# Kernel tuning notes

Hardware: AMD Instinct MI355X
Metric: run time of the kernel (lower is better)

## Reference

```python
import jax, jax.numpy as jnp
import numpy as np

N = 1024          # number of junctions
H = 1024          # heatmap height
W = 1024          # heatmap width
NUM_SAMPLES = 64  # samples along each candidate segment (torch_sampler)
DETECT_THRESH = 0.5
INLIER_THRESH = 0.99


def setup_inputs() -> dict:
    key = jax.random.key(0)
    k1, k2 = jax.random.split(key)
    # junctions are (h, w) float coordinates inside the image
    junctions = jax.random.uniform(k1, (N, 2), dtype=jnp.float32) * (H - 1)
    heatmap = jax.random.uniform(k2, (H, W), dtype=jnp.float32)
    return {"junctions": junctions, "heatmap": heatmap}


def _bilinear_sample(heatmap, ch, cw):
    """SOLD2 detect_bilinear: gather 4 corners, bilinear weights. ch/cw: [N,N,S]."""
    hf = jnp.floor(ch); hc = jnp.ceil(ch)
    wf = jnp.floor(cw); wc = jnp.ceil(cw)
    hfi = hf.astype(jnp.int32); hci = hc.astype(jnp.int32)
    wfi = wf.astype(jnp.int32); wci = wc.astype(jnp.int32)
    return (heatmap[hfi, wfi] * (hc - ch) * (wc - cw)
          + heatmap[hfi, wci] * (hc - ch) * (cw - wf)
          + heatmap[hci, wfi] * (ch - hf) * (wc - cw)
          + heatmap[hci, wci] * (ch - hf) * (cw - wf))


def reference(junctions, heatmap):
    n = junctions.shape[0]
    Hh, Ww = heatmap.shape
    t = jnp.linspace(0.0, 1.0, NUM_SAMPLES, dtype=jnp.float32)  # [S]
    # cand_samples[i, j, s] = junc[i] * t[s] + junc[j] * (1 - t[s])  (start=i, end=j)
    ch = junctions[:, None, 0:1] * t + junctions[None, :, 0:1] * (1.0 - t)  # [N,N,S]
    cw = junctions[:, None, 1:2] * t + junctions[None, :, 1:2] * (1.0 - t)  # [N,N,S]
    ch = jnp.clip(ch, 0.0, Hh - 1)
    cw = jnp.clip(cw, 0.0, Ww - 1)
    feat = _bilinear_sample(heatmap, ch, cw)                    # [N,N,S]
    mean_feat = feat.mean(axis=-1)                              # [N,N]
    inlier_ratio = (feat > DETECT_THRESH).astype(jnp.float32).mean(axis=-1)
    # candidate map: strict upper triangle (torch.triu(ones, diagonal=1))
    cand_mask = jnp.triu(jnp.ones((n, n), dtype=bool), k=1)
    detected = (mean_feat > DETECT_THRESH) & (inlier_ratio >= INLIER_THRESH) & cand_mask
    line_map = (detected | detected.T).astype(jnp.int32)        # symmetric line map
    return line_map, mean_feat
```

## Files before the change

### kernel.cpp

```cpp
#include <hip/hip_runtime.h>

#define NJ 1024
#define DETECT 0.5f
#define RESCUE 0.4975f

__device__ __forceinline__ float sample_t(int s) {
    return (s == 63) ? 1.0f : (float)s * (1.0f / 63.0f);
}

__device__ __forceinline__ void exact_pair(const float2 ja, const float2 jb,
                                           const float* __restrict__ heat,
                                           float& mean_o, float& min_o)
{
    float acc = 0.0f;
    float mn  = __builtin_inff();
    for (int s = 0; s < 64; ++s) {
        const float t  = sample_t(s);
        const float om = 1.0f - t;
        float ch = __fadd_rn(__fmul_rn(ja.x, t), __fmul_rn(jb.x, om));
        float cw = __fadd_rn(__fmul_rn(ja.y, t), __fmul_rn(jb.y, om));
        ch = fminf(fmaxf(ch, 0.0f), 1023.0f);
        cw = fminf(fmaxf(cw, 0.0f), 1023.0f);
        const float hf = floorf(ch), hc = ceilf(ch);
        const float wf = floorf(cw), wc = ceilf(cw);
        const int hfi = (int)hf, hci = (int)hc;
        const int wfi = (int)wf, wci = (int)wc;
        const float a00 = heat[(hfi << 10) + wfi];
        const float a01 = heat[(hfi << 10) + wci];
        const float a10 = heat[(hci << 10) + wfi];
        const float a11 = heat[(hci << 10) + wci];
        const float t1 = __fmul_rn(__fmul_rn(a00, __fsub_rn(hc, ch)), __fsub_rn(wc, cw));
        const float t2 = __fmul_rn(__fmul_rn(a01, __fsub_rn(hc, ch)), __fsub_rn(cw, wf));
        const float t3 = __fmul_rn(__fmul_rn(a10, __fsub_rn(ch, hf)), __fsub_rn(wc, cw));
        const float t4 = __fmul_rn(__fmul_rn(a11, __fsub_rn(ch, hf)), __fsub_rn(cw, wf));
        const float feat = __fadd_rn(__fadd_rn(__fadd_rn(t1, t2), t3), t4);
        acc += feat;
        mn = fminf(mn, feat);
    }
    mean_o = acc * (1.0f / 64.0f);
    min_o  = mn;
}

__global__ __launch_bounds__(256) void pack_kernel(
    const float* __restrict__ heat, uint4* __restrict__ packed4,
    const float* __restrict__ junc,
    float* __restrict__ line_out, float* __restrict__ mean_out)
{
    const int idx = blockIdx.x * 256 + threadIdx.x;
    const int h = idx >> 8;
    const int w4 = (idx & 255) << 2;
    const int hn = (h < 1023) ? h + 1 : 1023;
    const float* r0 = heat + (h  << 10);
    const float* r1 = heat + (hn << 10);
    const float4 a = *(const float4*)(r0 + w4);
    const float4 b = *(const float4*)(r1 + w4);
    const int wnext = (w4 + 4 <= 1023) ? w4 + 4 : 1023;
    const float a4 = r0[wnext];
    const float b4 = r1[wnext];

    const float av[5] = {a.x, a.y, a.z, a.w, a4};
    const float bv[5] = {b.x, b.y, b.z, b.w, b4};
    unsigned int out[4];
    #pragma unroll
    for (int u = 0; u < 4; ++u) {
        const unsigned int c0 = (unsigned int)__float2int_rn(av[u]     * 255.0f);
        const unsigned int c1 = (unsigned int)__float2int_rn(av[u + 1] * 255.0f);
        const unsigned int c2 = (unsigned int)__float2int_rn(bv[u]     * 255.0f);
        const unsigned int c3 = (unsigned int)__float2int_rn(bv[u + 1] * 255.0f);
        out[u] = c0 | (c1 << 8) | (c2 << 16) | (c3 << 24);
    }
    packed4[idx] = make_uint4(out[0], out[1], out[2], out[3]);

    if (threadIdx.x == 0) {
        const int r = blockIdx.x;
        const float2 jr = ((const float2*)junc)[r];
        float mean, mnv;
        exact_pair(jr, jr, heat, mean, mnv);
        const int p = (r << 10) + r;
        mean_out[p] = mean;
        line_out[p] = 0.0f;
    }
}

__global__ __launch_bounds__(256) void sold2_thread_kernel(
    const float* __restrict__ junc,
    const float* __restrict__ heat,
    const unsigned int* __restrict__ packed,
    float* __restrict__ line_out,
    float* __restrict__ mean_out)
{
    const int q = blockIdx.x * 256 + threadIdx.x;
    const int r = q >> 9;
    const int c = (q & 511) + 1;
    const int j = (r + c) & 1023;

    const float2 jr  = ((const float2*)junc)[r];
    const float2 jjc = ((const float2*)junc)[j];

    float acc = 0.0f;
    float mn  = __builtin_inff();

    #pragma unroll
    for (int s0 = 0; s0 < 64; s0 += 16) {
        float chv[16], cwv[16];
        unsigned int cv[16];
        #pragma unroll
        for (int u = 0; u < 16; ++u) {
            const int s = s0 + u;
            const float t  = sample_t(s);
            const float om = 1.0f - t;
            float ch = __fadd_rn(__fmul_rn(jr.x, t), __fmul_rn(jjc.x, om));
            float cw = __fadd_rn(__fmul_rn(jr.y, t), __fmul_rn(jjc.y, om));
            ch = fminf(fmaxf(ch, 0.0f), 1023.0f);
            cw = fminf(fmaxf(cw, 0.0f), 1023.0f);
            chv[u] = ch;
            cwv[u] = cw;
            const int hfi = (int)ch;
            const int wfi = (int)cw;
            cv[u] = packed[(hfi << 10) + wfi];
        }
        #pragma unroll
        for (int u = 0; u < 16; ++u) {
            const float ch = chv[u], cw = cwv[u];
            const float hf = floorf(ch), hc = ceilf(ch);
            const float wf = floorf(cw), wc = ceilf(cw);
            const float wh0 = hc - ch, wh1 = ch - hf;
            const float ww0 = wc - cw, ww1 = cw - wf;
            const unsigned int cc = cv[u];
            const float a00 = (float)(cc & 0xffu);
            const float a01 = (float)((cc >> 8) & 0xffu);
            const float a10 = (float)((cc >> 16) & 0xffu);
            const float a11 = (float)(cc >> 24);
            const float feat = a00 * (wh0 * ww0) + a01 * (wh0 * ww1)
                             + a10 * (wh1 * ww0) + a11 * (wh1 * ww1);
            acc += feat;
            mn = fminf(mn, feat);
        }
    }

    float mean = acc * (1.0f / (255.0f * 64.0f));
    const float mns = mn * (1.0f / 255.0f);

    bool det = false;
    if ((mns > RESCUE) && (mean > RESCUE)) {
        float mn2;
        exact_pair(jr, jjc, heat, mean, mn2);
        det = (mean > DETECT) && (mn2 > DETECT);
    }

    const int p1 = (r << 10) + j;
    mean_out[p1] = mean;
    line_out[p1] = det ? 1.0f : 0.0f;
}

__global__ __launch_bounds__(256) void mirror_kernel(
    float* __restrict__ line_out, float* __restrict__ mean_out)
{
    __shared__ float lm[64][65];
    __shared__ float mm[64][65];
    const int bi = blockIdx.x >> 4;
    const int bj = blockIdx.x & 15;

    const int D = ((bj - bi) << 6) & 1023;
    if (D >= 63 && D <= 449) return;

    const int tx = threadIdx.x & 63;
    const int g  = threadIdx.x >> 6;

    #pragma unroll
    for (int k = 0; k < 16; ++k) {
        const int b = (g << 4) + k;
        const int src = ((bj << 6) + b) * 1024 + (bi << 6) + tx;
        lm[b][tx] = line_out[src];
        mm[b][tx] = mean_out[src];
    }
    __syncthreads();

    #pragma unroll
    for (int k = 0; k < 16; ++k) {
        const int a = (g << 4) + k;
        const int i = (bi << 6) + a;
        const int j = (bj << 6) + tx;
        const int d = (j - i) & 1023;
        if (d >= 513) {
            const int dst = i * 1024 + j;
            line_out[dst] = lm[tx][a];
            mean_out[dst] = mm[tx][a];
        }
    }
}

extern "C" void kernel_launch(void* const* d_in, const int* in_sizes, int n_in,
                              void* d_out, int out_size, void* d_ws, size_t ws_size,
                              hipStream_t stream) {
    const float* junc = (const float*)d_in[0];
    const float* heat = (const float*)d_in[1];
    float* line_out = (float*)d_out;
    float* mean_out = line_out + NJ * NJ;

    unsigned int* packed = (unsigned int*)d_ws;
    pack_kernel<<<1024, 256, 0, stream>>>(heat, (uint4*)packed, junc,
                                          line_out, mean_out);

    sold2_thread_kernel<<<2048, 256, 0, stream>>>(junc, heat, packed,
                                                  line_out, mean_out);

    mirror_kernel<<<256, 256, 0, stream>>>(line_out, mean_out);
}
```

Before: 212.7 us.

## Fuse pack, pair evaluation and mirroring into one cooperative grid-synced kernel

Merges the packing, band evaluation and mirror kernels into a single cooperative launch that uses a grid-wide barrier between packing the heatmap and evaluating junction pairs. Each pair thread now writes both (r,j) and (j,r) directly, which removes the separate shared-memory transpose pass. The diagonal is spread across threads instead of running on one thread per block, and each fused thread handles two rows. The cost is scattered transposed stores and a grid-sync that needs all 1024 blocks resident, with a non-cooperative fallback path if the launch fails.

```diff
diff --git a/kernel.cpp b/kernel.cpp
--- a/kernel.cpp
+++ b/kernel.cpp
@@ -1,4 +1,7 @@
 #include <hip/hip_runtime.h>
+#include <hip/hip_cooperative_groups.h>
+
+namespace cg = cooperative_groups;
 
 #define NJ 1024
 #define DETECT 0.5f
@@ -41,12 +44,9 @@
     min_o  = mn;
 }
 
-__global__ __launch_bounds__(256) void pack_kernel(
-    const float* __restrict__ heat, uint4* __restrict__ packed4,
-    const float* __restrict__ junc,
-    float* __restrict__ line_out, float* __restrict__ mean_out)
-{
-    const int idx = blockIdx.x * 256 + threadIdx.x;
+__device__ __forceinline__ void pack4(const float* __restrict__ heat,
+                                      uint4* __restrict__ packed4, int idx)
+{
     const int h = idx >> 8;
     const int w4 = (idx & 255) << 2;
     const int hn = (h < 1023) ? h + 1 : 1023;
@@ -70,30 +70,16 @@
         out[u] = c0 | (c1 << 8) | (c2 << 16) | (c3 << 24);
     }
     packed4[idx] = make_uint4(out[0], out[1], out[2], out[3]);
-
-    if (threadIdx.x == 0) {
-        const int r = blockIdx.x;
-        const float2 jr = ((const float2*)junc)[r];
-        float mean, mnv;
-        exact_pair(jr, jr, heat, mean, mnv);
-        const int p = (r << 10) + r;
-        mean_out[p] = mean;
-        line_out[p] = 0.0f;
-    }
-}
-
-__global__ __launch_bounds__(256) void sold2_thread_kernel(
-    const float* __restrict__ junc,
-    const float* __restrict__ heat,
-    const unsigned int* __restrict__ packed,
-    float* __restrict__ line_out,
-    float* __restrict__ mean_out)
-{
-    const int q = blockIdx.x * 256 + threadIdx.x;
-    const int r = q >> 9;
-    const int c = (q & 511) + 1;
+}
+
+__device__ __forceinline__ void do_pair(const float* __restrict__ junc,
+                                        const float* __restrict__ heat,
+                                        const unsigned int* __restrict__ packed,
+                                        float* __restrict__ line_out,
+                                        float* __restrict__ mean_out,
+                                        int r, int c)
+{
     const int j = (r + c) & 1023;
-
     const float2 jr  = ((const float2*)junc)[r];
     const float2 jjc = ((const float2*)junc)[j];
 
@@ -148,46 +134,66 @@
         det = (mean > DETECT) && (mn2 > DETECT);
     }
 
+    const float lv = det ? 1.0f : 0.0f;
     const int p1 = (r << 10) + j;
+    const int p2 = (j << 10) + r;
     mean_out[p1] = mean;
-    line_out[p1] = det ? 1.0f : 0.0f;
-}
-
-__global__ __launch_bounds__(256) void mirror_kernel(
+    mean_out[p2] = mean;
+    line_out[p1] = lv;
+    line_out[p2] = lv;
+}
+
+__device__ __forceinline__ void do_diag(const float* __restrict__ junc,
+                                        const float* __restrict__ heat,
+                                        float* __restrict__ line_out,
+                                        float* __restrict__ mean_out, int r)
+{
+    const float2 jr = ((const float2*)junc)[r];
+    float mean, mnv;
+    exact_pair(jr, jr, heat, mean, mnv);
+    const int p = (r << 10) + r;
+    mean_out[p] = mean;
+    line_out[p] = 0.0f;
+}
+
+__global__ __launch_bounds__(256, 4) void sold2_fused_kernel(
+    const float* __restrict__ junc, const float* __restrict__ heat,
+    unsigned int* __restrict__ packed,
     float* __restrict__ line_out, float* __restrict__ mean_out)
 {
-    __shared__ float lm[64][65];
-    __shared__ float mm[64][65];
-    const int bi = blockIdx.x >> 4;
-    const int bj = blockIdx.x & 15;
-
-    const int D = ((bj - bi) << 6) & 1023;
-    if (D >= 63 && D <= 449) return;
-
-    const int tx = threadIdx.x & 63;
-    const int g  = threadIdx.x >> 6;
-
-    #pragma unroll
-    for (int k = 0; k < 16; ++k) {
-        const int b = (g << 4) + k;
-        const int src = ((bj << 6) + b) * 1024 + (bi << 6) + tx;
-        lm[b][tx] = line_out[src];
-        mm[b][tx] = mean_out[src];
-    }
-    __syncthreads();
-
-    #pragma unroll
-    for (int k = 0; k < 16; ++k) {
-        const int a = (g << 4) + k;
-        const int i = (bi << 6) + a;
-        const int j = (bj << 6) + tx;
-        const int d = (j - i) & 1023;
-        if (d >= 513) {
-            const int dst = i * 1024 + j;
-            line_out[dst] = lm[tx][a];
-            mean_out[dst] = mm[tx][a];
-        }
-    }
+    const int q = blockIdx.x * 256 + threadIdx.x;
+
+    pack4(heat, (uint4*)packed, q);
+    if (q < NJ) do_diag(junc, heat, line_out, mean_out, q);
+
+    __threadfence();
+    cg::this_grid().sync();
+
+    #pragma unroll 1
+    for (int half = 0; half < 2; ++half) {
+        const int r = (q >> 9) | (half << 9);
+        const int c = (q & 511) + 1;
+        do_pair(junc, heat, packed, line_out, mean_out, r, c);
+    }
+}
+
+__global__ __launch_bounds__(256) void pack_diag_kernel(
+    const float* __restrict__ heat, uint4* __restrict__ packed4,
+    const float* __restrict__ junc,
+    float* __restrict__ line_out, float* __restrict__ mean_out)
+{
+    const int q = blockIdx.x * 256 + threadIdx.x;
+    pack4(heat, packed4, q);
+    if (q < NJ) do_diag(junc, heat, line_out, mean_out, q);
+}
+
+__global__ __launch_bounds__(256) void band_kernel(
+    const float* __restrict__ junc, const float* __restrict__ heat,
+    const unsigned int* __restrict__ packed,
+    float* __restrict__ line_out, float* __restrict__ mean_out)
+{
+    const int q = blockIdx.x * 256 + threadIdx.x;
+    do_pair(junc, heat, packed, line_out, mean_out, q >> 9, (q & 511) + 1);
 }
 
 extern "C" void kernel_launch(void* const* d_in, const int* in_sizes, int n_in,
@@ -197,13 +203,17 @@
     const float* heat = (const float*)d_in[1];
     float* line_out = (float*)d_out;
     float* mean_out = line_out + NJ * NJ;
-
     unsigned int* packed = (unsigned int*)d_ws;
-    pack_kernel<<<1024, 256, 0, stream>>>(heat, (uint4*)packed, junc,
-                                          line_out, mean_out);
-
-    sold2_thread_kernel<<<2048, 256, 0, stream>>>(junc, heat, packed,
-                                                  line_out, mean_out);
-
-    mirror_kernel<<<256, 256, 0, stream>>>(line_out, mean_out);
-}
+
+    void* args[] = {(void*)&junc, (void*)&heat, (void*)&packed,
+                    (void*)&line_out, (void*)&mean_out};
+    hipError_t err = hipLaunchCooperativeKernel(
+        (const void*)sold2_fused_kernel, dim3(1024), dim3(256), args, 0, stream);
+
+    if (err != hipSuccess) {
+        pack_diag_kernel<<<1024, 256, 0, stream>>>(heat, (uint4*)packed, junc,
+                                                   line_out, mean_out);
+        band_kernel<<<2048, 256, 0, stream>>>(junc, heat, packed,
+                                              line_out, mean_out);
+    }
+}
```

Measured after the change: 425.8 us. 100% more time.
